# Kernel tuning notes

Hardware: AMD Instinct MI355X
Metric: run time of the kernel (lower is better)

The kernel has to match this reference:

```python
import jax, jax.numpy as jnp
import numpy as np

N, E = 100000, 1600000
IN_DIM, HID, NCLS = 64, 128, 18
BATCH, K = 8, 5000


def setup_inputs() -> dict:
    key = jax.random.key(0)
    ks = jax.random.split(key, 9)
    features = jax.random.normal(ks[0], (N, IN_DIM), dtype=jnp.float32)
    src = jax.random.randint(ks[1], (E,), 0, N, dtype=jnp.int32)
    dst = jax.random.randint(ks[2], (E,), 0, N, dtype=jnp.int32)
    def glorot(k, shape):
        lim = float(np.sqrt(6.0 / (shape[0] + shape[1])))
        return jax.random.uniform(k, shape, jnp.float32, -lim, lim)
    W1 = glorot(ks[3], (IN_DIM, HID)); b1 = jnp.zeros((HID,), jnp.float32)
    W2 = glorot(ks[4], (HID, HID));    b2 = jnp.zeros((HID,), jnp.float32)
    W3 = glorot(ks[5], (K * HID, NCLS)); b3 = jnp.zeros((NCLS,), jnp.float32)
    return {"features": features, "src": src, "dst": dst,
            "W1": W1, "b1": b1, "W2": W2, "b2": b2, "W3": W3, "b3": b3}


def reference(features, src, dst, W1, b1, W2, b2, W3, b3):
    n = features.shape[0]
    ones = jnp.ones(src.shape[0], features.dtype)
    out_deg = jax.ops.segment_sum(ones, src, num_segments=n)
    in_deg = jax.ops.segment_sum(ones, dst, num_segments=n)
    norm_src = jnp.clip(out_deg, 1.0) ** -0.5  # DGL norm='both'
    norm_dst = jnp.clip(in_deg, 1.0) ** -0.5

    def gconv(x, W, b, act):
        h = (x @ W) * norm_src[:, None]          # transform then normalize src
        agg = jax.ops.segment_sum(h[src], dst, num_segments=n)  # gather+scatter-add
        agg = agg * norm_dst[:, None] + b
        return jax.nn.relu(agg) if act else agg

    h = gconv(features, W1, b1, True)   # [N, HID]
    h = gconv(h, W2, b2, True)          # [N, HID]

    # global_sort_pool: equal-sized graphs of N//BATCH nodes, top-K by last channel
    n_per = n // BATCH
    hb = h.reshape(BATCH, n_per, HID)
    _, idx = jax.lax.top_k(hb[..., -1], K)                  # [B, K] descending
    topk = jnp.take_along_axis(hb, idx[..., None], axis=1)  # [B, K, HID]
    pooled = topk.reshape(BATCH, K * HID)

    return pooled @ W3 + b3  # [B, NCLS]
```

## Files before the change

kernel.cpp:

```cpp
#include <hip/hip_runtime.h>
#include <cstdint>
#include <cstddef>

#define N_NODES 100000
#define N_EDGES 1600000
#define IN_DIM  64
#define HID     128
#define NCLS    18
#define BATCH   8
#define TOPK    5000
#define NPER    12500
#define SORTN   16384
#define SORTC   2048

#define BSHIFT  9
#define BNODES  (1 << BSHIFT)
#define NBUCK   ((N_NODES + BNODES - 1) / BNODES)
#define CHUNK   8192


__global__ __launch_bounds__(256) void k_degrees(const int* __restrict__ src,
                                                 const int* __restrict__ dst,
                                                 int* __restrict__ degS,
                                                 int* __restrict__ degD) {
    int e = blockIdx.x * 256 + threadIdx.x;
    if (e < N_EDGES) {
        atomicAdd(&degS[src[e]], 1);
        atomicAdd(&degD[dst[e]], 1);
    }
}

__global__ __launch_bounds__(256) void k_norms(const int* __restrict__ degS,
                                               const int* __restrict__ degD,
                                               float* __restrict__ normS,
                                               float* __restrict__ normD) {
    int i = blockIdx.x * 256 + threadIdx.x;
    if (i < N_NODES) {
        normS[i] = 1.0f / sqrtf((float)max(degS[i], 1));
        normD[i] = 1.0f / sqrtf((float)max(degD[i], 1));
    }
}


__global__ __launch_bounds__(1024) void k_scanA(const int* __restrict__ degD,
                                                int* __restrict__ blockSums) {
    __shared__ int lds[1024];
    int i = blockIdx.x * 1024 + threadIdx.x;
    lds[threadIdx.x] = (i < N_NODES) ? degD[i] : 0;
    __syncthreads();
    for (int s = 512; s > 0; s >>= 1) {
        if (threadIdx.x < s) lds[threadIdx.x] += lds[threadIdx.x + s];
        __syncthreads();
    }
    if (threadIdx.x == 0) blockSums[blockIdx.x] = lds[0];
}

__global__ void k_scanB(const int* __restrict__ blockSums, int* __restrict__ blockOff,
                        int nblocks) {
    if (threadIdx.x == 0 && blockIdx.x == 0) {
        int run = 0;
        for (int b = 0; b < nblocks; ++b) { blockOff[b] = run; run += blockSums[b]; }
        blockOff[nblocks] = run;
    }
}

__global__ __launch_bounds__(1024) void k_scanC(const int* __restrict__ degD,
                                                const int* __restrict__ blockOff,
                                                int* __restrict__ row_ptr) {
    __shared__ int lds[1024];
    int i = blockIdx.x * 1024 + threadIdx.x;
    int v = (i < N_NODES) ? degD[i] : 0;
    lds[threadIdx.x] = v;
    __syncthreads();
    for (int s = 1; s < 1024; s <<= 1) {
        int t = (threadIdx.x >= (unsigned)s) ? lds[threadIdx.x - s] : 0;
        __syncthreads();
        lds[threadIdx.x] += t;
        __syncthreads();
    }
    if (i < N_NODES) {
        int excl = lds[threadIdx.x] - v + blockOff[blockIdx.x];
        row_ptr[i] = excl;
    }
    if (i == 0) row_ptr[N_NODES] = blockOff[gridDim.x];
}


__global__ void k_binit(const int* __restrict__ row_ptr, int* __restrict__ bucketCursor) {
    int b = blockIdx.x * 256 + threadIdx.x;
    if (b < NBUCK) bucketCursor[b] = row_ptr[b << BSHIFT];
}

__global__ __launch_bounds__(256) void k_bin(const int* __restrict__ src,
                                             const int* __restrict__ dst,
                                             int* __restrict__ bucketCursor,
                                             unsigned* __restrict__ binbuf) {
    __shared__ int cnt[NBUCK];
    __shared__ int gbase[NBUCK];
    __shared__ int cnt2[NBUCK];
    const int base = blockIdx.x * CHUNK;
    const int end  = min(base + CHUNK, N_EDGES);
    for (int b = threadIdx.x; b < NBUCK; b += 256) { cnt[b] = 0; cnt2[b] = 0; }
    __syncthreads();
    for (int e = base + threadIdx.x; e < end; e += 256)
        atomicAdd(&cnt[dst[e] >> BSHIFT], 1);
    __syncthreads();
    for (int b = threadIdx.x; b < NBUCK; b += 256)
        if (cnt[b] > 0) gbase[b] = atomicAdd(&bucketCursor[b], cnt[b]);
    __syncthreads();
    for (int e = base + threadIdx.x; e < end; e += 256) {
        int d = dst[e];
        int b = d >> BSHIFT;
        int off = atomicAdd(&cnt2[b], 1);
        unsigned packed = ((unsigned)(d & (BNODES - 1)) << 17) | (unsigned)src[e];
        binbuf[gbase[b] + off] = packed;
    }
}

__global__ __launch_bounds__(256) void k_scatter(const unsigned* __restrict__ binbuf,
                                                 const int* __restrict__ row_ptr,
                                                 int* __restrict__ ssrc) {
    __shared__ int cur[BNODES];
    const int nodeBase = blockIdx.x << BSHIFT;
    for (int t = threadIdx.x; t < BNODES; t += 256) {
        int node = nodeBase + t;
        cur[t] = (node < N_NODES) ? row_ptr[node] : 0;
    }
    __syncthreads();
    const int beg = row_ptr[nodeBase];
    const int end = row_ptr[min(nodeBase + BNODES, N_NODES)];
    for (int e = beg + threadIdx.x; e < end; e += 256) {
        unsigned v = binbuf[e];
        int dl = (int)(v >> 17);
        int s  = (int)(v & 0x1FFFFu);
        int pos = atomicAdd(&cur[dl], 1);
        ssrc[pos] = s;
    }
}


#define BMT 64
#define BKT 32

template<int KDIM>
__global__ __launch_bounds__(256) void k_gemm_rt(const float* __restrict__ X,
                                                 const float* __restrict__ W,
                                                 const float* __restrict__ normS,
                                                 float* __restrict__ out) {
    __shared__ float xs[BMT][BKT + 4];
    __shared__ float ws[BKT * HID];

    const int tid = threadIdx.x;
    const int tx = tid & 31;
    const int ty = tid >> 5;
    const int col0 = tx * 4;
    const int row0 = ty * 8;
    const int rt = blockIdx.x * BMT;

    float acc[8][4];
    #pragma unroll
    for (int r = 0; r < 8; ++r)
        #pragma unroll
        for (int c = 0; c < 4; ++c) acc[r][c] = 0.f;

    for (int k0 = 0; k0 < KDIM; k0 += BKT) {
        __syncthreads();
        {
            const float4* wsrc = (const float4*)(W + (size_t)k0 * HID);
            #pragma unroll
            for (int i = tid; i < BKT * HID / 4; i += 256)
                ((float4*)ws)[i] = wsrc[i];
        }
        {
            #pragma unroll
            for (int i = tid; i < BMT * BKT / 4; i += 256) {
                int row = i >> 3;
                int kq  = i & 7;
                int gr  = rt + row;
                float4 v = make_float4(0.f, 0.f, 0.f, 0.f);
                if (gr < N_NODES)
                    v = *(const float4*)(X + (size_t)gr * KDIM + k0 + kq * 4);
                *(float4*)&xs[row][kq * 4] = v;
            }
        }
        __syncthreads();

        #pragma unroll 4
        for (int k = 0; k < BKT; ++k) {
            float4 b = *(const float4*)&ws[k * HID + col0];
            float a[8];
            #pragma unroll
            for (int r = 0; r < 8; ++r) a[r] = xs[row0 + r][k];
            #pragma unroll
            for (int r = 0; r < 8; ++r) {
                acc[r][0] += a[r] * b.x;
                acc[r][1] += a[r] * b.y;
                acc[r][2] += a[r] * b.z;
                acc[r][3] += a[r] * b.w;
            }
        }
    }

    #pragma unroll
    for (int r = 0; r < 8; ++r) {
        int gr = rt + row0 + r;
        if (gr < N_NODES) {
            float s = normS[gr];
            float4 o = make_float4(acc[r][0] * s, acc[r][1] * s, acc[r][2] * s, acc[r][3] * s);
            *(float4*)(out + (size_t)gr * HID + col0) = o;
        }
    }
}


__global__ __launch_bounds__(256) void k_agg(const float* __restrict__ hs,
                                             const int* __restrict__ row_ptr,
                                             const int* __restrict__ ssrc,
                                             const float* __restrict__ normD,
                                             const float* __restrict__ bias,
                                             float* __restrict__ out,
                                             float* __restrict__ keys) {
    int node = blockIdx.x * 8 + (threadIdx.x >> 5);
    int lane = threadIdx.x & 31;
    if (node >= N_NODES) return;
    int beg = row_ptr[node], end = row_ptr[node + 1];
    float4 acc = make_float4(0.f, 0.f, 0.f, 0.f);
    int e = beg;
    for (; e + 1 < end; e += 2) {
        int s0 = ssrc[e], s1 = ssrc[e + 1];
        float4 v0 = ((const float4*)(hs + (size_t)s0 * HID))[lane];
        float4 v1 = ((const float4*)(hs + (size_t)s1 * HID))[lane];
        acc.x += v0.x; acc.y += v0.y; acc.z += v0.z; acc.w += v0.w;
        acc.x += v1.x; acc.y += v1.y; acc.z += v1.z; acc.w += v1.w;
    }
    if (e < end) {
        int s0 = ssrc[e];
        float4 v0 = ((const float4*)(hs + (size_t)s0 * HID))[lane];
        acc.x += v0.x; acc.y += v0.y; acc.z += v0.z; acc.w += v0.w;
    }
    float nrm = normD[node];
    float4 bb = *(const float4*)(bias + lane * 4);
    float4 o;
    o.x = fmaxf(acc.x * nrm + bb.x, 0.f);
    o.y = fmaxf(acc.y * nrm + bb.y, 0.f);
    o.z = fmaxf(acc.z * nrm + bb.z, 0.f);
    o.w = fmaxf(acc.w * nrm + bb.w, 0.f);
    *(float4*)(out + (size_t)node * HID + lane * 4) = o;
    if (keys != nullptr && lane == 31) keys[node] = o.w;
}


__global__ __launch_bounds__(256) void k_sort_init(const float* __restrict__ keys,
                                                   unsigned long long* __restrict__ arr) {
    int i = blockIdx.x * 256 + threadIdx.x;
    if (i >= BATCH * SORTN) return;
    int g = i >> 14;
    int l = i & (SORTN - 1);
    unsigned long long c;
    if (l < NPER) {
        unsigned u = __float_as_uint(keys[g * NPER + l]);
        unsigned s = (u & 0x80000000u) ? ~u : (u | 0x80000000u);
        unsigned d = ~s;
        c = ((unsigned long long)d << 32) | (unsigned)l;
    } else {
        c = 0xFFFFFFFFFFFFFFFFull;
    }
    arr[i] = c;
}

__global__ __launch_bounds__(1024) void k_sort_local_full(unsigned long long* __restrict__ arr) {
    __shared__ unsigned long long lds[SORTC];
    const int base  = blockIdx.x * SORTC;
    const int gbase = base & (SORTN - 1);
    lds[threadIdx.x]        = arr[base + threadIdx.x];
    lds[threadIdx.x + 1024] = arr[base + threadIdx.x + 1024];
    __syncthreads();
    for (int k = 2; k <= SORTC; k <<= 1) {
        for (int j = k >> 1; j > 0; j >>= 1) {
            int t = threadIdx.x;
            int i = ((t & ~(j - 1)) << 1) | (t & (j - 1));
            bool up = (((gbase + i) & k) == 0);
            unsigned long long a = lds[i], b = lds[i + j];
            if ((a > b) == up) { lds[i] = b; lds[i + j] = a; }
            __syncthreads();
        }
    }
    arr[base + threadIdx.x]        = lds[threadIdx.x];
    arr[base + threadIdx.x + 1024] = lds[threadIdx.x + 1024];
}

__global__ __launch_bounds__(256) void k_sort_global(unsigned long long* __restrict__ arr,
                                                     int k, int j) {
    int tg = blockIdx.x * 256 + threadIdx.x;
    if (tg >= BATCH * (SORTN / 2)) return;
    int g = tg >> 13;
    int t = tg & (SORTN / 2 - 1);
    int i = ((t & ~(j - 1)) << 1) | (t & (j - 1));
    bool up = ((i & k) == 0);
    unsigned long long* p = arr + (size_t)g * SORTN;
    unsigned long long a = p[i], b = p[i + j];
    if ((a > b) == up) { p[i] = b; p[i + j] = a; }
}

__global__ __launch_bounds__(1024) void k_sort_local_tail(unsigned long long* __restrict__ arr,
                                                          int k) {
    __shared__ unsigned long long lds[SORTC];
    const int base  = blockIdx.x * SORTC;
    const int gbase = base & (SORTN - 1);
    lds[threadIdx.x]        = arr[base + threadIdx.x];
    lds[threadIdx.x + 1024] = arr[base + threadIdx.x + 1024];
    __syncthreads();
    for (int j = SORTC >> 1; j > 0; j >>= 1) {
        int t = threadIdx.x;
        int i = ((t & ~(j - 1)) << 1) | (t & (j - 1));
        bool up = (((gbase + i) & k) == 0);
        unsigned long long a = lds[i], b = lds[i + j];
        if ((a > b) == up) { lds[i] = b; lds[i + j] = a; }
        __syncthreads();
    }
    arr[base + threadIdx.x]        = lds[threadIdx.x];
    arr[base + threadIdx.x + 1024] = lds[threadIdx.x + 1024];
}

__global__ __launch_bounds__(256) void k_sort_emit(const unsigned long long* __restrict__ arr,
                                                   int* __restrict__ topk_idx) {
    int i = blockIdx.x * 256 + threadIdx.x;
    if (i >= BATCH * TOPK) return;
    int b = i / TOPK;
    int k = i - b * TOPK;
    topk_idx[i] = (int)(arr[(size_t)b * SORTN + k] & 0xFFFFFFFFull);
}


__global__ void k_outinit(const float* __restrict__ b3, float* __restrict__ out) {
    int i = threadIdx.x;
    if (i < BATCH * NCLS) out[i] = b3[i % NCLS];
}

#define KPB 100

__global__ __launch_bounds__(128) void k_final(const float* __restrict__ h2,
                                               const int* __restrict__ topk_idx,
                                               const float* __restrict__ W3,
                                               float* __restrict__ out) {
    __shared__ float red[128 * NCLS];
    const int b = blockIdx.x / (TOPK / KPB);
    const int chunk = blockIdx.x % (TOPK / KPB);
    const int j = threadIdx.x;
    float acc[NCLS];
    #pragma unroll
    for (int c = 0; c < NCLS; ++c) acc[c] = 0.f;
    const int k0 = chunk * KPB;
    for (int k = k0; k < k0 + KPB; ++k) {
        int node = b * NPER + topk_idx[b * TOPK + k];
        float h = h2[(size_t)node * HID + j];
        const float* wrow = W3 + (size_t)(k * HID + j) * NCLS;
        #pragma unroll
        for (int c = 0; c < NCLS; ++c) acc[c] += h * wrow[c];
    }
    #pragma unroll
    for (int c = 0; c < NCLS; ++c) red[j * NCLS + c] = acc[c];
    __syncthreads();
    for (int s = 64; s > 0; s >>= 1) {
        if (j < s) {
            #pragma unroll
            for (int c = 0; c < NCLS; ++c) red[j * NCLS + c] += red[(j + s) * NCLS + c];
        }
        __syncthreads();
    }
    if (j < NCLS) atomicAdd(&out[b * NCLS + j], red[j]);
}


extern "C" void kernel_launch(void* const* d_in, const int* in_sizes, int n_in,
                              void* d_out, int out_size, void* d_ws, size_t ws_size,
                              hipStream_t stream) {
    const float* features = (const float*)d_in[0];
    const int*   src      = (const int*)d_in[1];
    const int*   dst      = (const int*)d_in[2];
    const float* W1       = (const float*)d_in[3];
    const float* b1       = (const float*)d_in[4];
    const float* W2       = (const float*)d_in[5];
    const float* b2       = (const float*)d_in[6];
    const float* W3       = (const float*)d_in[7];
    const float* b3       = (const float*)d_in[8];
    float* out = (float*)d_out;

    char* p = (char*)d_ws;
    auto carve = [&](size_t bytes) -> void* {
        void* r = (void*)p;
        p += (bytes + 511) & ~(size_t)511;
        return r;
    };
    int*   degS      = (int*)carve((size_t)N_NODES * 4);
    int*   degD      = (int*)carve((size_t)N_NODES * 4);
    float* normS     = (float*)carve((size_t)N_NODES * 4);
    float* normD     = (float*)carve((size_t)N_NODES * 4);
    int*   row_ptr   = (int*)carve((size_t)(N_NODES + 1) * 4);
    int*   bucketCursor = (int*)carve((size_t)NBUCK * 4);
    int*   blockSums = (int*)carve(1024 * 4);
    int*   blockOff  = (int*)carve(1024 * 4);
    int*   ssrc      = (int*)carve((size_t)N_EDGES * 4);
    unsigned* binbuf = (unsigned*)carve((size_t)N_EDGES * 4);
    float* keys      = (float*)carve((size_t)N_NODES * 4);
    int*   topk_idx  = (int*)carve((size_t)BATCH * TOPK * 4);
    unsigned long long* sortbuf = (unsigned long long*)carve((size_t)BATCH * SORTN * 8);
    float* bufA      = (float*)carve((size_t)N_NODES * HID * 4);
    float* bufB      = (float*)carve((size_t)N_NODES * HID * 4);

    const int EB = (N_EDGES + 255) / 256;
    const int NB = (N_NODES + 255) / 256;
    const int SB = (N_NODES + 1023) / 1024;
    const int GB = (N_NODES + BMT - 1) / BMT;
    const int BB = (N_EDGES + CHUNK - 1) / CHUNK;

    hipMemsetAsync(degS, 0, (size_t)N_NODES * 4, stream);
    hipMemsetAsync(degD, 0, (size_t)N_NODES * 4, stream);

    k_degrees<<<EB, 256, 0, stream>>>(src, dst, degS, degD);
    k_norms<<<NB, 256, 0, stream>>>(degS, degD, normS, normD);
    k_scanA<<<SB, 1024, 0, stream>>>(degD, blockSums);
    k_scanB<<<1, 64, 0, stream>>>(blockSums, blockOff, SB);
    k_scanC<<<SB, 1024, 0, stream>>>(degD, blockOff, row_ptr);

    k_binit<<<1, 256, 0, stream>>>(row_ptr, bucketCursor);
    k_bin<<<BB, 256, 0, stream>>>(src, dst, bucketCursor, binbuf);
    k_scatter<<<NBUCK, 256, 0, stream>>>(binbuf, row_ptr, ssrc);

    k_gemm_rt<IN_DIM><<<GB, 256, 0, stream>>>(features, W1, normS, bufA);
    k_agg<<<(N_NODES + 7) / 8, 256, 0, stream>>>(bufA, row_ptr, ssrc, normD, b1, bufB, nullptr);
    k_gemm_rt<HID><<<GB, 256, 0, stream>>>(bufB, W2, normS, bufA);
    k_agg<<<(N_NODES + 7) / 8, 256, 0, stream>>>(bufA, row_ptr, ssrc, normD, b2, bufB, keys);

    const int NCHUNK = BATCH * SORTN / SORTC;
    const int GCE    = (BATCH * (SORTN / 2) + 255) / 256;
    k_sort_init<<<(BATCH * SORTN + 255) / 256, 256, 0, stream>>>(keys, sortbuf);
    k_sort_local_full<<<NCHUNK, 1024, 0, stream>>>(sortbuf);
    k_sort_global<<<GCE, 256, 0, stream>>>(sortbuf, 4096, 2048);
    k_sort_local_tail<<<NCHUNK, 1024, 0, stream>>>(sortbuf, 4096);
    k_sort_global<<<GCE, 256, 0, stream>>>(sortbuf, 8192, 4096);
    k_sort_global<<<GCE, 256, 0, stream>>>(sortbuf, 8192, 2048);
    k_sort_local_tail<<<NCHUNK, 1024, 0, stream>>>(sortbuf, 8192);
    k_sort_global<<<GCE, 256, 0, stream>>>(sortbuf, 16384, 8192);
    k_sort_global<<<GCE, 256, 0, stream>>>(sortbuf, 16384, 4096);
    k_sort_global<<<GCE, 256, 0, stream>>>(sortbuf, 16384, 2048);
    k_sort_local_tail<<<NCHUNK, 1024, 0, stream>>>(sortbuf, 16384);
    k_sort_emit<<<(BATCH * TOPK + 255) / 256, 256, 0, stream>>>(sortbuf, topk_idx);

    k_outinit<<<1, 256, 0, stream>>>(b3, out);
    k_final<<<BATCH * (TOPK / KPB), 128, 0, stream>>>(bufB, topk_idx, W3, out);
}
```

Measured before the change: 721.3 us.

## Replace global-atomic degree counting with bucketed binning and per-bucket LDS histograms

Per-node degree counting used global atomics over all edges, followed by a multi-kernel prefix scan to build row_ptr. Now edges are first counted per bucket of 512 nodes using LDS atomics, then binned by dst and by src into bucket-contiguous buffers. Per-bucket kernels compute degrees with LDS histograms, derive the norms, and build row_ptr through an in-block scan. This removes the 3.2M random global atomics but adds an extra binning pass over src and one more edge-sized buffer.

```diff
diff --git a/kernel.cpp b/kernel.cpp
--- a/kernel.cpp
+++ b/kernel.cpp
@@ -19,81 +19,43 @@
 #define CHUNK   8192
 
 
-__global__ __launch_bounds__(256) void k_degrees(const int* __restrict__ src,
-                                                 const int* __restrict__ dst,
-                                                 int* __restrict__ degS,
-                                                 int* __restrict__ degD) {
-    int e = blockIdx.x * 256 + threadIdx.x;
-    if (e < N_EDGES) {
-        atomicAdd(&degS[src[e]], 1);
-        atomicAdd(&degD[dst[e]], 1);
-    }
-}
-
-__global__ __launch_bounds__(256) void k_norms(const int* __restrict__ degS,
-                                               const int* __restrict__ degD,
-                                               float* __restrict__ normS,
-                                               float* __restrict__ normD) {
-    int i = blockIdx.x * 256 + threadIdx.x;
-    if (i < N_NODES) {
-        normS[i] = 1.0f / sqrtf((float)max(degS[i], 1));
-        normD[i] = 1.0f / sqrtf((float)max(degD[i], 1));
-    }
-}
-
-
-__global__ __launch_bounds__(1024) void k_scanA(const int* __restrict__ degD,
-                                                int* __restrict__ blockSums) {
-    __shared__ int lds[1024];
-    int i = blockIdx.x * 1024 + threadIdx.x;
-    lds[threadIdx.x] = (i < N_NODES) ? degD[i] : 0;
-    __syncthreads();
-    for (int s = 512; s > 0; s >>= 1) {
-        if (threadIdx.x < s) lds[threadIdx.x] += lds[threadIdx.x + s];
-        __syncthreads();
-    }
-    if (threadIdx.x == 0) blockSums[blockIdx.x] = lds[0];
-}
-
-__global__ void k_scanB(const int* __restrict__ blockSums, int* __restrict__ blockOff,
-                        int nblocks) {
+__global__ __launch_bounds__(256) void k_bcount(const int* __restrict__ src,
+                                                const int* __restrict__ dst,
+                                                int* __restrict__ bcntS,
+                                                int* __restrict__ bcntD) {
+    __shared__ int cs[NBUCK], cd[NBUCK];
+    for (int b = threadIdx.x; b < NBUCK; b += 256) { cs[b] = 0; cd[b] = 0; }
+    __syncthreads();
+    const int base = blockIdx.x * CHUNK;
+    const int end  = min(base + CHUNK, N_EDGES);
+    for (int e = base + threadIdx.x; e < end; e += 256) {
+        atomicAdd(&cs[src[e] >> BSHIFT], 1);
+        atomicAdd(&cd[dst[e] >> BSHIFT], 1);
+    }
+    __syncthreads();
+    for (int b = threadIdx.x; b < NBUCK; b += 256) {
+        if (cs[b]) atomicAdd(&bcntS[b], cs[b]);
+        if (cd[b]) atomicAdd(&bcntD[b], cd[b]);
+    }
+}
+
+__global__ void k_bscan(const int* __restrict__ bcntS, const int* __restrict__ bcntD,
+                        int* __restrict__ baseS, int* __restrict__ baseD,
+                        int* __restrict__ curS, int* __restrict__ curD) {
     if (threadIdx.x == 0 && blockIdx.x == 0) {
-        int run = 0;
-        for (int b = 0; b < nblocks; ++b) { blockOff[b] = run; run += blockSums[b]; }
-        blockOff[nblocks] = run;
-    }
-}
-
-__global__ __launch_bounds__(1024) void k_scanC(const int* __restrict__ degD,
-                                                const int* __restrict__ blockOff,
-                                                int* __restrict__ row_ptr) {
-    __shared__ int lds[1024];
-    int i = blockIdx.x * 1024 + threadIdx.x;
-    int v = (i < N_NODES) ? degD[i] : 0;
-    lds[threadIdx.x] = v;
-    __syncthreads();
-    for (int s = 1; s < 1024; s <<= 1) {
-        int t = (threadIdx.x >= (unsigned)s) ? lds[threadIdx.x - s] : 0;
-        __syncthreads();
-        lds[threadIdx.x] += t;
-        __syncthreads();
-    }
-    if (i < N_NODES) {
-        int excl = lds[threadIdx.x] - v + blockOff[blockIdx.x];
-        row_ptr[i] = excl;
-    }
-    if (i == 0) row_ptr[N_NODES] = blockOff[gridDim.x];
-}
-
-
-__global__ void k_binit(const int* __restrict__ row_ptr, int* __restrict__ bucketCursor) {
-    int b = blockIdx.x * 256 + threadIdx.x;
-    if (b < NBUCK) bucketCursor[b] = row_ptr[b << BSHIFT];
-}
+        int rs = 0, rd = 0;
+        for (int b = 0; b < NBUCK; ++b) {
+            baseS[b] = rs; curS[b] = rs; rs += bcntS[b];
+            baseD[b] = rd; curD[b] = rd; rd += bcntD[b];
+        }
+        baseS[NBUCK] = rs; baseD[NBUCK] = rd;
+    }
+}
+
 
 __global__ __launch_bounds__(256) void k_bin(const int* __restrict__ src,
                                              const int* __restrict__ dst,
-                                             int* __restrict__ bucketCursor,
+                                             int* __restrict__ cursorD,
                                              unsigned* __restrict__ binbuf) {
     __shared__ int cnt[NBUCK];
     __shared__ int gbase[NBUCK];
@@ -106,7 +68,7 @@
         atomicAdd(&cnt[dst[e] >> BSHIFT], 1);
     __syncthreads();
     for (int b = threadIdx.x; b < NBUCK; b += 256)
-        if (cnt[b] > 0) gbase[b] = atomicAdd(&bucketCursor[b], cnt[b]);
+        if (cnt[b] > 0) gbase[b] = atomicAdd(&cursorD[b], cnt[b]);
     __syncthreads();
     for (int e = base + threadIdx.x; e < end; e += 256) {
         int d = dst[e];
@@ -115,6 +77,82 @@
         unsigned packed = ((unsigned)(d & (BNODES - 1)) << 17) | (unsigned)src[e];
         binbuf[gbase[b] + off] = packed;
     }
+}
+
+__global__ __launch_bounds__(256) void k_bin_src(const int* __restrict__ src,
+                                                 int* __restrict__ cursorS,
+                                                 unsigned* __restrict__ sbin) {
+    __shared__ int cnt[NBUCK];
+    __shared__ int gbase[NBUCK];
+    __shared__ int cnt2[NBUCK];
+    const int base = blockIdx.x * CHUNK;
+    const int end  = min(base + CHUNK, N_EDGES);
+    for (int b = threadIdx.x; b < NBUCK; b += 256) { cnt[b] = 0; cnt2[b] = 0; }
+    __syncthreads();
+    for (int e = base + threadIdx.x; e < end; e += 256)
+        atomicAdd(&cnt[src[e] >> BSHIFT], 1);
+    __syncthreads();
+    for (int b = threadIdx.x; b < NBUCK; b += 256)
+        if (cnt[b] > 0) gbase[b] = atomicAdd(&cursorS[b], cnt[b]);
+    __syncthreads();
+    for (int e = base + threadIdx.x; e < end; e += 256) {
+        int s = src[e];
+        int b = s >> BSHIFT;
+        int off = atomicAdd(&cnt2[b], 1);
+        sbin[gbase[b] + off] = (unsigned)(s & (BNODES - 1));
+    }
+}
+
+
+__global__ __launch_bounds__(256) void k_histS(const unsigned* __restrict__ sbin,
+                                               const int* __restrict__ baseS,
+                                               float* __restrict__ normS) {
+    __shared__ int cnt[BNODES];
+    for (int t = threadIdx.x; t < BNODES; t += 256) cnt[t] = 0;
+    __syncthreads();
+    const int beg = baseS[blockIdx.x], end = baseS[blockIdx.x + 1];
+    for (int e = beg + threadIdx.x; e < end; e += 256)
+        atomicAdd(&cnt[sbin[e]], 1);
+    __syncthreads();
+    const int nodeBase = blockIdx.x << BSHIFT;
+    for (int t = threadIdx.x; t < BNODES; t += 256) {
+        int node = nodeBase + t;
+        if (node < N_NODES)
+            normS[node] = 1.0f / sqrtf((float)max(cnt[t], 1));
+    }
+}
+
+__global__ __launch_bounds__(256) void k_histD(const unsigned* __restrict__ binbuf,
+                                               const int* __restrict__ baseD,
+                                               float* __restrict__ normD,
+                                               int* __restrict__ row_ptr) {
+    __shared__ int cnt[BNODES];
+    __shared__ int tmp[BNODES];
+    for (int t = threadIdx.x; t < BNODES; t += 256) cnt[t] = 0;
+    __syncthreads();
+    const int beg = baseD[blockIdx.x], end = baseD[blockIdx.x + 1];
+    for (int e = beg + threadIdx.x; e < end; e += 256)
+        atomicAdd(&cnt[binbuf[e] >> 17], 1);
+    __syncthreads();
+    const int nodeBase = blockIdx.x << BSHIFT;
+    for (int t = threadIdx.x; t < BNODES; t += 256) {
+        int node = nodeBase + t;
+        if (node < N_NODES)
+            normD[node] = 1.0f / sqrtf((float)max(cnt[t], 1));
+    }
+    for (int s = 1; s < BNODES; s <<= 1) {
+        for (int t = threadIdx.x; t < BNODES; t += 256)
+            tmp[t] = (t >= s) ? cnt[t - s] + cnt[t] : cnt[t];
+        __syncthreads();
+        for (int t = threadIdx.x; t < BNODES; t += 256) cnt[t] = tmp[t];
+        __syncthreads();
+    }
+    for (int t = threadIdx.x; t < BNODES; t += 256) {
+        int node = nodeBase + t;
+        if (node < N_NODES)
+            row_ptr[node] = beg + ((t == 0) ? 0 : cnt[t - 1]);
+    }
+    if (blockIdx.x == 0 && threadIdx.x == 0) row_ptr[N_NODES] = N_EDGES;
 }
 
 __global__ __launch_bounds__(256) void k_scatter(const unsigned* __restrict__ binbuf,
@@ -392,39 +430,36 @@
         p += (bytes + 511) & ~(size_t)511;
         return r;
     };
-    int*   degS      = (int*)carve((size_t)N_NODES * 4);
-    int*   degD      = (int*)carve((size_t)N_NODES * 4);
     float* normS     = (float*)carve((size_t)N_NODES * 4);
     float* normD     = (float*)carve((size_t)N_NODES * 4);
     int*   row_ptr   = (int*)carve((size_t)(N_NODES + 1) * 4);
-    int*   bucketCursor = (int*)carve((size_t)NBUCK * 4);
-    int*   blockSums = (int*)carve(1024 * 4);
-    int*   blockOff  = (int*)carve(1024 * 4);
+    int*   bcntS     = (int*)carve((size_t)NBUCK * 4);
+    int*   bcntD     = (int*)carve((size_t)NBUCK * 4);
+    int*   baseS     = (int*)carve((size_t)(NBUCK + 1) * 4);
+    int*   baseD     = (int*)carve((size_t)(NBUCK + 1) * 4);
+    int*   curS      = (int*)carve((size_t)NBUCK * 4);
+    int*   curD      = (int*)carve((size_t)NBUCK * 4);
     int*   ssrc      = (int*)carve((size_t)N_EDGES * 4);
     unsigned* binbuf = (unsigned*)carve((size_t)N_EDGES * 4);
+    unsigned* sbin   = (unsigned*)carve((size_t)N_EDGES * 4);
     float* keys      = (float*)carve((size_t)N_NODES * 4);
     int*   topk_idx  = (int*)carve((size_t)BATCH * TOPK * 4);
     unsigned long long* sortbuf = (unsigned long long*)carve((size_t)BATCH * SORTN * 8);
     float* bufA      = (float*)carve((size_t)N_NODES * HID * 4);
     float* bufB      = (float*)carve((size_t)N_NODES * HID * 4);
 
-    const int EB = (N_EDGES + 255) / 256;
-    const int NB = (N_NODES + 255) / 256;
-    const int SB = (N_NODES + 1023) / 1024;
     const int GB = (N_NODES + BMT - 1) / BMT;
     const int BB = (N_EDGES + CHUNK - 1) / CHUNK;
 
-    hipMemsetAsync(degS, 0, (size_t)N_NODES * 4, stream);
-    hipMemsetAsync(degD, 0, (size_t)N_NODES * 4, stream);
-
-    k_degrees<<<EB, 256, 0, stream>>>(src, dst, degS, degD);
-    k_norms<<<NB, 256, 0, stream>>>(degS, degD, normS, normD);
-    k_scanA<<<SB, 1024, 0, stream>>>(degD, blockSums);
-    k_scanB<<<1, 64, 0, stream>>>(blockSums, blockOff, SB);
-    k_scanC<<<SB, 1024, 0, stream>>>(degD, blockOff, row_ptr);
-
-    k_binit<<<1, 256, 0, stream>>>(row_ptr, bucketCursor);
-    k_bin<<<BB, 256, 0, stream>>>(src, dst, bucketCursor, binbuf);
+    hipMemsetAsync(bcntS, 0, (size_t)NBUCK * 4, stream);
+    hipMemsetAsync(bcntD, 0, (size_t)NBUCK * 4, stream);
+
+    k_bcount<<<BB, 256, 0, stream>>>(src, dst, bcntS, bcntD);
+    k_bscan<<<1, 64, 0, stream>>>(bcntS, bcntD, baseS, baseD, curS, curD);
+    k_bin<<<BB, 256, 0, stream>>>(src, dst, curD, binbuf);
+    k_bin_src<<<BB, 256, 0, stream>>>(src, curS, sbin);
+    k_histS<<<NBUCK, 256, 0, stream>>>(sbin, baseS, normS);
+    k_histD<<<NBUCK, 256, 0, stream>>>(binbuf, baseD, normD, row_ptr);
     k_scatter<<<NBUCK, 256, 0, stream>>>(binbuf, row_ptr, ssrc);
 
     k_gemm_rt<IN_DIM><<<GB, 256, 0, stream>>>(features, W1, normS, bufA);
```

New measurement: 650.3 us. 9.9% less time.
